# Optimization experiments

Measured on AMD Instinct MI355X. Metric: run time of the kernel, lower is better.

## Reference

```python
import jax, jax.numpy as jnp
import numpy as np

N, L, H, D_HEAD, P = 2, 1024, 8, 64, 1
DIM = H * D_HEAD


def setup_inputs() -> dict:
    key0 = jax.random.key(0)
    ks = jax.random.split(key0, 7)
    query = jax.random.normal(ks[0], (N, L, DIM), dtype=jnp.float32)
    key = jax.random.normal(ks[1], (N, L, DIM), dtype=jnp.float32)
    scale = 1.0 / np.sqrt(DIM)
    Wq = jax.random.normal(ks[2], (DIM, DIM), dtype=jnp.float32) * scale
    Wk = jax.random.normal(ks[3], (DIM, DIM), dtype=jnp.float32) * scale
    Wv = jax.random.normal(ks[4], (DIM, DIM), dtype=jnp.float32) * scale
    position_weight = jax.random.uniform(ks[5], (H, P, D_HEAD), dtype=jnp.float32) * 2 - 1
    position_bias = jax.random.uniform(ks[6], (H, D_HEAD), dtype=jnp.float32) * 2 - 1
    return {"query": query, "key": key, "Wq": Wq, "Wk": Wk, "Wv": Wv,
            "position_weight": position_weight, "position_bias": position_bias}


def _kernel_fn(x):
    # _log_exp_kernel: positive feature map log(1 + exp(x)) (softplus)
    return jax.nn.softplus(x)


def _causal_term(qf, kf, v):
    """Linear-complexity causal attention term.
    qf, kf: (N,H,L,d) feature-mapped query/key; v: (N,H,L,d) values.
    Returns numerator (N,H,L,d) and denominator (N,H,L)."""
    # cumulative key-value outer products: (N,H,L,d,d)
    kv = jnp.cumsum(jnp.einsum('nhkd,nhke->nhkde', kf, v), axis=2)
    num = jnp.einsum('nhqd,nhqde->nhqe', qf, kv)
    den = jnp.einsum('nhqd,nhqd->nhq', qf, jnp.cumsum(kf, axis=2))
    return num, den


def reference(query, key, Wq, Wk, Wv, position_weight, position_bias):
    n, lq, dim = query.shape
    lk = key.shape[1]
    h, p, d = position_weight.shape
    kernel = _kernel_fn
    # projections (torch Linear: x @ W.T), reshape to heads, transpose to (N,H,L,d)
    q = kernel((query @ Wq.T).reshape(n, lq, h, d)).transpose(0, 2, 1, 3)
    k = kernel((key @ Wk.T).reshape(n, lk, h, d)).transpose(0, 2, 1, 3)
    v = ((key @ Wv.T).reshape(n, lk, h, d)).transpose(0, 2, 1, 3)
    # default positions: arange, expanded to (N,L,P)
    qpos = jnp.broadcast_to(jnp.arange(lq, dtype=query.dtype)[None, :, None], (n, lq, p))
    kpos = jnp.broadcast_to(jnp.arange(lk, dtype=key.dtype)[None, :, None], (n, lk, p))
    pq = jnp.einsum('nlp,hpd->nhld', qpos, position_weight) \
         + jax.nn.sigmoid(position_bias)[None, :, None, :] * jnp.pi
    pk = jnp.einsum('nlp,hpd->nhld', kpos, position_weight)
    # three branches: cos, sin, plain (trig identity split of cos(pq - pk) RPE)
    num_c, den_c = _causal_term(q * jnp.cos(pq), k * jnp.cos(pk), v)
    num_s, den_s = _causal_term(q * jnp.sin(pq), k * jnp.sin(pk), v)
    num_p, den_p = _causal_term(q, k, v)
    num = num_c + num_s + num_p
    den = den_c + den_s + den_p
    attention = num / den[..., None]  # scaled=True
    return attention.transpose(0, 2, 1, 3).reshape(n, lq, dim)
```

## Files before the change

### kernel.cpp

```cpp
#include <hip/hip_runtime.h>
#include <hip/hip_bf16.h>

#define LSEQ   1024
#define NHEAD  8
#define DH     64
#define DIM    512
#define NHTOT  16
#define DF     192
#define LDB    68
#define LDQ    200
#define LDV    72

typedef __attribute__((ext_vector_type(8))) short short8;
typedef __attribute__((ext_vector_type(4))) float floatx4;

__device__ __forceinline__ float softplusf_(float x) {
    if (x > 20.f) return x;
    return log1pf(expf(x));
}
__device__ __forceinline__ unsigned short bf16_rne(float x) {
    unsigned int u = __float_as_uint(x);
    u += 0x7FFFu + ((u >> 16) & 1u);
    return (unsigned short)(u >> 16);
}
__device__ __forceinline__ float bf16_tof(unsigned short h) {
    return __uint_as_float(((unsigned int)h) << 16);
}

__global__ __launch_bounds__(256) void proj_kernel(
    const float* __restrict__ query, const float* __restrict__ key,
    const float* __restrict__ Wq, const float* __restrict__ Wk,
    const float* __restrict__ Wv,
    const float* __restrict__ pw, const float* __restrict__ pb,
    unsigned short* __restrict__ qf, unsigned short* __restrict__ kf,
    unsigned short* __restrict__ vbuf)
{
    const int mt  = blockIdx.x;
    const int ot  = blockIdx.y;
    const int sel = blockIdx.z;
    const int t   = threadIdx.x;

    const float* __restrict__ X = (sel == 0) ? query : key;
    const float* __restrict__ W = (sel == 0) ? Wq : (sel == 1) ? Wk : Wv;

    __shared__ unsigned short As[64 * LDB];
    __shared__ unsigned short Bs[64 * LDB];

    const int m0 = mt * 64, o0 = ot * 64;
    const int lane = t & 63, wave = t >> 6;
    const int quad = lane >> 4, l16 = lane & 15;
    const int wm = wave >> 1, wn = wave & 1;

    const int srow = t >> 2;
    const int sc16 = (t & 3) * 16;

    floatx4 acc[2][2];
    #pragma unroll
    for (int i = 0; i < 2; ++i)
        #pragma unroll
        for (int j = 0; j < 2; ++j) acc[i][j] = (floatx4){0.f, 0.f, 0.f, 0.f};

    float4 ax[4], bx4[4];
    #pragma unroll
    for (int i = 0; i < 4; ++i) {
        ax[i]  = *(const float4*)&X[(size_t)(m0 + srow) * DIM + sc16 + i * 4];
        bx4[i] = *(const float4*)&W[(size_t)(o0 + srow) * DIM + sc16 + i * 4];
    }

    for (int kt = 0; kt < DIM; kt += 64) {
        __syncthreads();
        {
            short8 a0, a1, b0, b1;
            #pragma unroll
            for (int i = 0; i < 2; ++i) {
                const float va[4] = {ax[i].x, ax[i].y, ax[i].z, ax[i].w};
                const float vb[4] = {bx4[i].x, bx4[i].y, bx4[i].z, bx4[i].w};
                #pragma unroll
                for (int j = 0; j < 4; ++j) {
                    a0[i * 4 + j] = (short)bf16_rne(va[j]);
                    b0[i * 4 + j] = (short)bf16_rne(vb[j]);
                }
            }
            #pragma unroll
            for (int i = 2; i < 4; ++i) {
                const float va[4] = {ax[i].x, ax[i].y, ax[i].z, ax[i].w};
                const float vb[4] = {bx4[i].x, bx4[i].y, bx4[i].z, bx4[i].w};
                #pragma unroll
                for (int j = 0; j < 4; ++j) {
                    a1[(i - 2) * 4 + j] = (short)bf16_rne(va[j]);
                    b1[(i - 2) * 4 + j] = (short)bf16_rne(vb[j]);
                }
            }
            *(short8*)&As[srow * LDB + sc16]     = a0;
            *(short8*)&As[srow * LDB + sc16 + 8] = a1;
            *(short8*)&Bs[srow * LDB + sc16]     = b0;
            *(short8*)&Bs[srow * LDB + sc16 + 8] = b1;
        }
        __syncthreads();

        if (kt + 64 < DIM) {
            #pragma unroll
            for (int i = 0; i < 4; ++i) {
                ax[i]  = *(const float4*)&X[(size_t)(m0 + srow) * DIM + kt + 64 + sc16 + i * 4];
                bx4[i] = *(const float4*)&W[(size_t)(o0 + srow) * DIM + kt + 64 + sc16 + i * 4];
            }
        }

        #pragma unroll
        for (int s = 0; s < 2; ++s) {
            short8 af[2], bf[2];
            #pragma unroll
            for (int mi = 0; mi < 2; ++mi)
                af[mi] = *(const short8*)&As[(wm * 32 + mi * 16 + l16) * LDB + s * 32 + quad * 8];
            #pragma unroll
            for (int ni = 0; ni < 2; ++ni)
                bf[ni] = *(const short8*)&Bs[(wn * 32 + ni * 16 + l16) * LDB + s * 32 + quad * 8];
            #pragma unroll
            for (int ni = 0; ni < 2; ++ni)
                #pragma unroll
                for (int mi = 0; mi < 2; ++mi)
                    acc[mi][ni] = __builtin_amdgcn_mfma_f32_16x16x32_bf16(af[mi], bf[ni], acc[mi][ni], 0, 0, 0);
        }
    }

    const int h = ot;
    const float PI_ = 3.14159265358979323846f;
    if (sel == 2) {
        #pragma unroll
        for (int mi = 0; mi < 2; ++mi)
            #pragma unroll
            for (int ni = 0; ni < 2; ++ni) {
                const int d = wn * 32 + ni * 16 + l16;
                #pragma unroll
                for (int r = 0; r < 4; ++r) {
                    const int m = m0 + wm * 32 + mi * 16 + quad * 4 + r;
                    const int n = m >> 10, l = m & (LSEQ - 1);
                    vbuf[(((size_t)(n * NHEAD + h)) * LSEQ + l) * DH + d] =
                        bf16_rne(acc[mi][ni][r]);
                }
            }
    } else {
        unsigned short* __restrict__ obuf = (sel == 0) ? qf : kf;
        #pragma unroll
        for (int ni = 0; ni < 2; ++ni) {
            const int d = wn * 32 + ni * 16 + l16;
            const float w = pw[h * DH + d];
            const float bias = (sel == 0) ? PI_ / (1.f + expf(-pb[h * DH + d])) : 0.f;
            #pragma unroll
            for (int mi = 0; mi < 2; ++mi)
                #pragma unroll
                for (int r = 0; r < 4; ++r) {
                    const int m = m0 + wm * 32 + mi * 16 + quad * 4 + r;
                    const int n = m >> 10, l = m & (LSEQ - 1);
                    const float val = softplusf_(acc[mi][ni][r]);
                    float sn, cs;
                    sincosf((float)l * w + bias, &sn, &cs);
                    const size_t ob = (((size_t)(n * NHEAD + h)) * LSEQ + l) * DF + d;
                    obuf[ob]            = bf16_rne(val);
                    obuf[ob + DH]       = bf16_rne(val * cs);
                    obuf[ob + 2 * DH]   = bf16_rne(val * sn);
                }
        }
    }
}

__global__ __launch_bounds__(256) void attn_kernel(
    const unsigned short* __restrict__ qf, const unsigned short* __restrict__ kf,
    const unsigned short* __restrict__ vbuf,
    float* __restrict__ outp)
{
    const int p  = blockIdx.x;
    const int nh = blockIdx.y;
    const int z  = blockIdx.z;
    const int lt = z ? (31 - p) : p;
    const int n  = nh >> 3;
    const int h  = nh & (NHEAD - 1);
    const int t  = threadIdx.x;
    const int lane = t & 63, wave = t >> 6;
    const int quad = lane >> 4, l16 = lane & 15;
    const int wm = wave >> 1, wn = wave & 1;

    __shared__ unsigned short qL[32 * LDQ];
    __shared__ unsigned short kL[64 * LDQ];
    __shared__ unsigned short vT[64 * LDV];
    __shared__ unsigned short scA[32 * LDV];
    __shared__ float denL[2][32];
    __shared__ float inv32[32];

    const size_t fbase = (size_t)nh * LSEQ;
    const int nkt = (lt >> 1) + 1;
    const int diag_kt = lt >> 1;

    #pragma unroll
    for (int i = 0; i < 6; ++i) {
        const int idx = i * 256 + t;
        const int r = idx / 48, c4 = (idx % 48) * 4;
        *(ushort4*)&qL[r * LDQ + c4] =
            *(const ushort4*)&qf[(fbase + lt * 32 + r) * DF + c4];
    }

    floatx4 accN[2];
    accN[0] = (floatx4){0.f, 0.f, 0.f, 0.f};
    accN[1] = (floatx4){0.f, 0.f, 0.f, 0.f};
    float den4[4] = {0.f, 0.f, 0.f, 0.f};

    for (int kt = 0; kt < nkt; ++kt) {
        #pragma unroll
        for (int i = 0; i < 12; ++i) {
            const int idx = i * 256 + t;
            const int r = idx / 48, c4 = (idx % 48) * 4;
            *(ushort4*)&kL[r * LDQ + c4] =
                *(const ushort4*)&kf[(fbase + kt * 64 + r) * DF + c4];
        }
        {
            const int col = t & 63, kq = (t >> 6) * 16;
            unsigned short vvv[16];
            #pragma unroll
            for (int j = 0; j < 16; ++j)
                vvv[j] = vbuf[(fbase + kt * 64 + kq + j) * DH + col];
            #pragma unroll
            for (int g = 0; g < 4; ++g) {
                ushort4 b;
                b.x = vvv[g * 4]; b.y = vvv[g * 4 + 1];
                b.z = vvv[g * 4 + 2]; b.w = vvv[g * 4 + 3];
                *(ushort4*)&vT[col * LDV + kq + g * 4] = b;
            }
        }
        __syncthreads();

        floatx4 accS[2];
        accS[0] = (floatx4){0.f, 0.f, 0.f, 0.f};
        accS[1] = (floatx4){0.f, 0.f, 0.f, 0.f};
        #pragma unroll
        for (int kk = 0; kk < 6; ++kk) {
            const short8 a = *(const short8*)&qL[(wm * 16 + l16) * LDQ + kk * 32 + quad * 8];
            #pragma unroll
            for (int ni = 0; ni < 2; ++ni) {
                const short8 b = *(const short8*)&kL[(wn * 32 + ni * 16 + l16) * LDQ + kk * 32 + quad * 8];
                accS[ni] = __builtin_amdgcn_mfma_f32_16x16x32_bf16(a, b, accS[ni], 0, 0, 0);
            }
        }

        const bool diag = (kt == diag_kt);
        #pragma unroll
        for (int ni = 0; ni < 2; ++ni) {
            const int kcolL = wn * 32 + ni * 16 + l16;
            const int kcolG = kt * 64 + kcolL;
            #pragma unroll
            for (int r = 0; r < 4; ++r) {
                const int lrowL = wm * 16 + quad * 4 + r;
                float sval = accS[ni][r];
                if (diag && kcolG > lt * 32 + lrowL) sval = 0.f;
                den4[r] += sval;
                scA[lrowL * LDV + kcolL] = bf16_rne(sval);
            }
        }
        __syncthreads();

        #pragma unroll
        for (int kk = 0; kk < 2; ++kk) {
            const short8 a = *(const short8*)&scA[(wm * 16 + l16) * LDV + kk * 32 + quad * 8];
            #pragma unroll
            for (int ni = 0; ni < 2; ++ni) {
                const short8 b = *(const short8*)&vT[(wn * 32 + ni * 16 + l16) * LDV + kk * 32 + quad * 8];
                accN[ni] = __builtin_amdgcn_mfma_f32_16x16x32_bf16(a, b, accN[ni], 0, 0, 0);
            }
        }
        __syncthreads();
    }

    #pragma unroll
    for (int r = 0; r < 4; ++r) {
        float s = den4[r];
        s += __shfl_xor(s, 1);
        s += __shfl_xor(s, 2);
        s += __shfl_xor(s, 4);
        s += __shfl_xor(s, 8);
        if (l16 == 0) denL[wn][wm * 16 + quad * 4 + r] = s;
    }
    __syncthreads();
    if (t < 32) inv32[t] = 1.f / (denL[0][t] + denL[1][t]);
    __syncthreads();

    #pragma unroll
    for (int ni = 0; ni < 2; ++ni) {
        const int e = wn * 32 + ni * 16 + l16;
        #pragma unroll
        for (int r = 0; r < 4; ++r) {
            const int row = wm * 16 + quad * 4 + r;
            outp[((size_t)n * LSEQ + lt * 32 + row) * DIM + h * DH + e] =
                accN[ni][r] * inv32[row];
        }
    }
}

extern "C" void kernel_launch(void* const* d_in, const int* in_sizes, int n_in,
                              void* d_out, int out_size, void* d_ws, size_t ws_size,
                              hipStream_t stream) {
    const float* query = (const float*)d_in[0];
    const float* key   = (const float*)d_in[1];
    const float* Wq    = (const float*)d_in[2];
    const float* Wk    = (const float*)d_in[3];
    const float* Wv    = (const float*)d_in[4];
    const float* pw    = (const float*)d_in[5];
    const float* pb    = (const float*)d_in[6];

    unsigned short* U = (unsigned short*)d_ws;
    unsigned short* qf   = U;
    unsigned short* kf   = U + 3145728;
    unsigned short* vbuf = U + 6291456;

    proj_kernel<<<dim3(32, 8, 3), 256, 0, stream>>>(
        query, key, Wq, Wk, Wv, pw, pb, qf, kf, vbuf);
    attn_kernel<<<dim3(16, 16, 2), 256, 0, stream>>>(
        qf, kf, vbuf, (float*)d_out);
}
```

Before: 118.8 us.

## Prefetch K/V tiles in registers, store V transposed, cheapen projection epilogue

The attention kernel now keeps Q fragments in registers and prefetches the next K tile and V tile into registers while MFMAs run on the current tile. The projection kernel writes V already transposed (staged through LDS), so attention no longer does scalar strided gathers to transpose V. The projection epilogue swaps per-element sincos for angle-addition recurrences and uses fast exp/log softplus and hardware packed bf16 conversion. The 1D grid remaps blocks so heads interleave. The trig recurrences and fast math introduce small numerical drift, and register prefetch raises register pressure.

```diff
diff --git a/kernel.cpp b/kernel.cpp
--- a/kernel.cpp
+++ b/kernel.cpp
@@ -1,30 +1,29 @@
 #include <hip/hip_runtime.h>
-#include <hip/hip_bf16.h>
 
 #define LSEQ   1024
 #define NHEAD  8
 #define DH     64
 #define DIM    512
-#define NHTOT  16
 #define DF     192
-#define LDB    68
+#define LDB    72
 #define LDQ    200
 #define LDV    72
 
 typedef __attribute__((ext_vector_type(8))) short short8;
 typedef __attribute__((ext_vector_type(4))) float floatx4;
 
-__device__ __forceinline__ float softplusf_(float x) {
-    if (x > 20.f) return x;
-    return log1pf(expf(x));
-}
 __device__ __forceinline__ unsigned short bf16_rne(float x) {
     unsigned int u = __float_as_uint(x);
     u += 0x7FFFu + ((u >> 16) & 1u);
     return (unsigned short)(u >> 16);
 }
-__device__ __forceinline__ float bf16_tof(unsigned short h) {
-    return __uint_as_float(((unsigned int)h) << 16);
+__device__ __forceinline__ unsigned int pk_bf16(float lo, float hi) {
+    unsigned int d;
+    asm("v_cvt_pk_bf16_f32 %0, %1, %2" : "=v"(d) : "v"(lo), "v"(hi));
+    return d;
+}
+__device__ __forceinline__ float softplus_fast(float x) {
+    return (x > 15.f) ? x : __logf(1.f + __expf(x));
 }
 
 __global__ __launch_bounds__(256) void proj_kernel(
@@ -70,31 +69,18 @@
     for (int kt = 0; kt < DIM; kt += 64) {
         __syncthreads();
         {
-            short8 a0, a1, b0, b1;
-            #pragma unroll
-            for (int i = 0; i < 2; ++i) {
-                const float va[4] = {ax[i].x, ax[i].y, ax[i].z, ax[i].w};
-                const float vb[4] = {bx4[i].x, bx4[i].y, bx4[i].z, bx4[i].w};
-                #pragma unroll
-                for (int j = 0; j < 4; ++j) {
-                    a0[i * 4 + j] = (short)bf16_rne(va[j]);
-                    b0[i * 4 + j] = (short)bf16_rne(vb[j]);
-                }
-            }
-            #pragma unroll
-            for (int i = 2; i < 4; ++i) {
-                const float va[4] = {ax[i].x, ax[i].y, ax[i].z, ax[i].w};
-                const float vb[4] = {bx4[i].x, bx4[i].y, bx4[i].z, bx4[i].w};
-                #pragma unroll
-                for (int j = 0; j < 4; ++j) {
-                    a1[(i - 2) * 4 + j] = (short)bf16_rne(va[j]);
-                    b1[(i - 2) * 4 + j] = (short)bf16_rne(vb[j]);
-                }
-            }
-            *(short8*)&As[srow * LDB + sc16]     = a0;
-            *(short8*)&As[srow * LDB + sc16 + 8] = a1;
-            *(short8*)&Bs[srow * LDB + sc16]     = b0;
-            *(short8*)&Bs[srow * LDB + sc16 + 8] = b1;
+            unsigned int ua[8], ub[8];
+            #pragma unroll
+            for (int i = 0; i < 4; ++i) {
+                ua[2*i]   = pk_bf16(ax[i].x, ax[i].y);
+                ua[2*i+1] = pk_bf16(ax[i].z, ax[i].w);
+                ub[2*i]   = pk_bf16(bx4[i].x, bx4[i].y);
+                ub[2*i+1] = pk_bf16(bx4[i].z, bx4[i].w);
+            }
+            *(uint4*)&As[srow * LDB + sc16]     = *(uint4*)&ua[0];
+            *(uint4*)&As[srow * LDB + sc16 + 8] = *(uint4*)&ua[4];
+            *(uint4*)&Bs[srow * LDB + sc16]     = *(uint4*)&ub[0];
+            *(uint4*)&Bs[srow * LDB + sc16 + 8] = *(uint4*)&ub[4];
         }
         __syncthreads();
 
@@ -125,7 +111,10 @@
 
     const int h = ot;
     const float PI_ = 3.14159265358979323846f;
+    const int n_ = m0 >> 10;
+
     if (sel == 2) {
+        __syncthreads();
         #pragma unroll
         for (int mi = 0; mi < 2; ++mi)
             #pragma unroll
@@ -133,33 +122,50 @@
                 const int d = wn * 32 + ni * 16 + l16;
                 #pragma unroll
                 for (int r = 0; r < 4; ++r) {
-                    const int m = m0 + wm * 32 + mi * 16 + quad * 4 + r;
-                    const int n = m >> 10, l = m & (LSEQ - 1);
-                    vbuf[(((size_t)(n * NHEAD + h)) * LSEQ + l) * DH + d] =
-                        bf16_rne(acc[mi][ni][r]);
+                    const int ml = wm * 32 + mi * 16 + quad * 4 + r;
+                    As[ml * LDB + d] = bf16_rne(acc[mi][ni][r]);
                 }
             }
+        __syncthreads();
+        const int d = t >> 2, mq = (t & 3) * 16;
+        const int l0 = m0 & (LSEQ - 1);
+        unsigned short col[16];
+        #pragma unroll
+        for (int j = 0; j < 16; ++j) col[j] = As[(mq + j) * LDB + d];
+        unsigned short* dst = &vbuf[((size_t)(n_ * NHEAD + h) * DH + d) * LSEQ + l0 + mq];
+        *(short8*)&dst[0] = *(short8*)&col[0];
+        *(short8*)&dst[8] = *(short8*)&col[8];
     } else {
         unsigned short* __restrict__ obuf = (sel == 0) ? qf : kf;
         #pragma unroll
         for (int ni = 0; ni < 2; ++ni) {
             const int d = wn * 32 + ni * 16 + l16;
             const float w = pw[h * DH + d];
-            const float bias = (sel == 0) ? PI_ / (1.f + expf(-pb[h * DH + d])) : 0.f;
-            #pragma unroll
-            for (int mi = 0; mi < 2; ++mi)
+            const float bias = (sel == 0) ? PI_ / (1.f + __expf(-pb[h * DH + d])) : 0.f;
+            float s1, c1; sincosf(w, &s1, &c1);
+            const float c2  = c1*c1 - s1*s1,  s2  = 2.f*c1*s1;
+            const float c4  = c2*c2 - s2*s2,  s4  = 2.f*c2*s2;
+            const float c8  = c4*c4 - s4*s4,  s8  = 2.f*c4*s4;
+            const float c16 = c8*c8 - s8*s8,  s16 = 2.f*c8*s8;
+            const int lb = (m0 & (LSEQ - 1)) + wm * 32 + quad * 4;
+            float sb, cb; sincosf((float)lb * w + bias, &sb, &cb);
+            #pragma unroll
+            for (int mi = 0; mi < 2; ++mi) {
+                float cc = cb, ss = sb;
                 #pragma unroll
                 for (int r = 0; r < 4; ++r) {
-                    const int m = m0 + wm * 32 + mi * 16 + quad * 4 + r;
-                    const int n = m >> 10, l = m & (LSEQ - 1);
-                    const float val = softplusf_(acc[mi][ni][r]);
-                    float sn, cs;
-                    sincosf((float)l * w + bias, &sn, &cs);
-                    const size_t ob = (((size_t)(n * NHEAD + h)) * LSEQ + l) * DF + d;
-                    obuf[ob]            = bf16_rne(val);
-                    obuf[ob + DH]       = bf16_rne(val * cs);
-                    obuf[ob + 2 * DH]   = bf16_rne(val * sn);
+                    const int l = lb + mi * 16 + r;
+                    const float val = softplus_fast(acc[mi][ni][r]);
+                    const size_t ob = ((size_t)(n_ * NHEAD + h) * LSEQ + l) * DF + d;
+                    obuf[ob]          = bf16_rne(val);
+                    obuf[ob + DH]     = bf16_rne(val * cc);
+                    obuf[ob + 2*DH]   = bf16_rne(val * ss);
+                    const float nc = cc * c1 - ss * s1;
+                    ss = ss * c1 + cc * s1; cc = nc;
                 }
+                const float nb = cb * c16 - sb * s16;
+                sb = sb * c16 + cb * s16; cb = nb;
+            }
         }
     }
 }
@@ -169,9 +175,10 @@
     const unsigned short* __restrict__ vbuf,
     float* __restrict__ outp)
 {
-    const int p  = blockIdx.x;
-    const int nh = blockIdx.y;
-    const int z  = blockIdx.z;
+    const int b  = blockIdx.x;
+    const int nh = (b & 7) * 2 + ((b >> 3) & 1);
+    const int p  = (b >> 4) & 15;
+    const int z  = b >> 8;
     const int lt = z ? (31 - p) : p;
     const int n  = nh >> 3;
     const int h  = nh & (NHEAD - 1);
@@ -180,7 +187,6 @@
     const int quad = lane >> 4, l16 = lane & 15;
     const int wm = wave >> 1, wn = wave & 1;
 
-    __shared__ unsigned short qL[32 * LDQ];
     __shared__ unsigned short kL[64 * LDQ];
     __shared__ unsigned short vT[64 * LDV];
     __shared__ unsigned short scA[32 * LDV];
@@ -191,13 +197,37 @@
     const int nkt = (lt >> 1) + 1;
     const int diag_kt = lt >> 1;
 
-    #pragma unroll
-    for (int i = 0; i < 6; ++i) {
-        const int idx = i * 256 + t;
-        const int r = idx / 48, c4 = (idx % 48) * 4;
-        *(ushort4*)&qL[r * LDQ + c4] =
-            *(const ushort4*)&qf[(fbase + lt * 32 + r) * DF + c4];
-    }
+    short8 qreg[6];
+    {
+        const unsigned short* qrow = &qf[(fbase + lt * 32 + wm * 16 + l16) * DF + quad * 8];
+        #pragma unroll
+        for (int kk = 0; kk < 6; ++kk)
+            qreg[kk] = *(const short8*)&qrow[kk * 32];
+    }
+
+    int kr[6], kc[6];
+    #pragma unroll
+    for (int c = 0; c < 6; ++c) {
+        const int idx = c * 256 + t;
+        kr[c] = idx / 24;
+        kc[c] = (idx % 24) * 8;
+    }
+    const unsigned short* kfb = &kf[fbase * DF];
+    const int ve = t >> 2, vk = (t & 3) * 16;
+    const unsigned short* vfb = &vbuf[((size_t)nh * DH + ve) * LSEQ + vk];
+
+    short8 kpre[6], vpre[2];
+    #pragma unroll
+    for (int c = 0; c < 6; ++c)
+        kpre[c] = *(const short8*)&kfb[(size_t)kr[c] * DF + kc[c]];
+    vpre[0] = *(const short8*)&vfb[0];
+    vpre[1] = *(const short8*)&vfb[8];
+    #pragma unroll
+    for (int c = 0; c < 6; ++c)
+        *(short8*)&kL[kr[c] * LDQ + kc[c]] = kpre[c];
+    *(short8*)&vT[ve * LDV + vk]     = vpre[0];
+    *(short8*)&vT[ve * LDV + vk + 8] = vpre[1];
+    __syncthreads();
 
     floatx4 accN[2];
     accN[0] = (floatx4){0.f, 0.f, 0.f, 0.f};
@@ -205,39 +235,25 @@
     float den4[4] = {0.f, 0.f, 0.f, 0.f};
 
     for (int kt = 0; kt < nkt; ++kt) {
-        #pragma unroll
-        for (int i = 0; i < 12; ++i) {
-            const int idx = i * 256 + t;
-            const int r = idx / 48, c4 = (idx % 48) * 4;
-            *(ushort4*)&kL[r * LDQ + c4] =
-                *(const ushort4*)&kf[(fbase + kt * 64 + r) * DF + c4];
-        }
-        {
-            const int col = t & 63, kq = (t >> 6) * 16;
-            unsigned short vvv[16];
-            #pragma unroll
-            for (int j = 0; j < 16; ++j)
-                vvv[j] = vbuf[(fbase + kt * 64 + kq + j) * DH + col];
-            #pragma unroll
-            for (int g = 0; g < 4; ++g) {
-                ushort4 b;
-                b.x = vvv[g * 4]; b.y = vvv[g * 4 + 1];
-                b.z = vvv[g * 4 + 2]; b.w = vvv[g * 4 + 3];
-                *(ushort4*)&vT[col * LDV + kq + g * 4] = b;
-            }
-        }
-        __syncthreads();
+        const bool pf = (kt + 1 < nkt);
+        if (pf) {
+            const size_t koff = (size_t)(kt + 1) * 64 * DF;
+            #pragma unroll
+            for (int c = 0; c < 6; ++c)
+                kpre[c] = *(const short8*)&kfb[koff + (size_t)kr[c] * DF + kc[c]];
+            vpre[0] = *(const short8*)&vfb[(kt + 1) * 64];
+            vpre[1] = *(const short8*)&vfb[(kt + 1) * 64 + 8];
+        }
 
         floatx4 accS[2];
         accS[0] = (floatx4){0.f, 0.f, 0.f, 0.f};
         accS[1] = (floatx4){0.f, 0.f, 0.f, 0.f};
         #pragma unroll
         for (int kk = 0; kk < 6; ++kk) {
-            const short8 a = *(const short8*)&qL[(wm * 16 + l16) * LDQ + kk * 32 + quad * 8];
             #pragma unroll
             for (int ni = 0; ni < 2; ++ni) {
-                const short8 b = *(const short8*)&kL[(wn * 32 + ni * 16 + l16) * LDQ + kk * 32 + quad * 8];
-                accS[ni] = __builtin_amdgcn_mfma_f32_16x16x32_bf16(a, b, accS[ni], 0, 0, 0);
+                const short8 bfr = *(const short8*)&kL[(wn * 32 + ni * 16 + l16) * LDQ + kk * 32 + quad * 8];
+                accS[ni] = __builtin_amdgcn_mfma_f32_16x16x32_bf16(qreg[kk], bfr, accS[ni], 0, 0, 0);
             }
         }
 
@@ -262,11 +278,20 @@
             const short8 a = *(const short8*)&scA[(wm * 16 + l16) * LDV + kk * 32 + quad * 8];
             #pragma unroll
             for (int ni = 0; ni < 2; ++ni) {
-                const short8 b = *(const short8*)&vT[(wn * 32 + ni * 16 + l16) * LDV + kk * 32 + quad * 8];
-                accN[ni] = __builtin_amdgcn_mfma_f32_16x16x32_bf16(a, b, accN[ni], 0, 0, 0);
-            }
-        }
-        __syncthreads();
+                const short8 bfr = *(const short8*)&vT[(wn * 32 + ni * 16 + l16) * LDV + kk * 32 + quad * 8];
+                accN[ni] = __builtin_amdgcn_mfma_f32_16x16x32_bf16(a, bfr, accN[ni], 0, 0, 0);
+            }
+        }
+        __syncthreads();
+
+        if (pf) {
+            #pragma unroll
+            for (int c = 0; c < 6; ++c)
+                *(short8*)&kL[kr[c] * LDQ + kc[c]] = kpre[c];
+            *(short8*)&vT[ve * LDV + vk]     = vpre[0];
+            *(short8*)&vT[ve * LDV + vk + 8] = vpre[1];
+            __syncthreads();
+        }
     }
 
     #pragma unroll
@@ -312,6 +337,6 @@
 
     proj_kernel<<<dim3(32, 8, 3), 256, 0, stream>>>(
         query, key, Wq, Wk, Wv, pw, pb, qf, kf, vbuf);
-    attn_kernel<<<dim3(16, 16, 2), 256, 0, stream>>>(
+    attn_kernel<<<dim3(512, 1, 1), 256, 0, stream>>>(
         qf, kf, vbuf, (float*)d_out);
 }
```

After: 105.4 us, median of 2. 11.3% less time.
